# Optimization experiments

Hardware: AMD Instinct MI355X
Metric: run time of the kernel (lower is better)

The kernel has to match this reference:

```python
import jax, jax.numpy as jnp
import numpy as np

N_E = 8192
DIM = 256
BETA = 0.25


def _l2norm(x, eps=1e-12):
    # matches F.normalize(p=2, dim=-1): x / max(||x||, eps)
    n = jnp.sqrt(jnp.sum(x * x, axis=-1, keepdims=True))
    return x / jnp.maximum(n, eps)


def setup_inputs() -> dict:
    key = jax.random.key(0)
    k1, k2 = jax.random.split(key)
    z = jax.random.normal(k1, (8, 1024, DIM), dtype=jnp.float32)
    embedding_weight = jax.random.normal(k2, (N_E, DIM), dtype=jnp.float32)
    return {"z": z, "embedding_weight": embedding_weight}


def reference(z, embedding_weight):
    z = _l2norm(z)                                   # [B,S,D]
    zf = z.reshape(-1, DIM)                          # [N,D]
    embed_norm = _l2norm(embedding_weight)           # [n_e,D]
    # d = ||z||^2 + ||e||^2 - 2 z.e  -> [N, n_e]
    d = (jnp.sum(zf * zf, axis=1, keepdims=True)
         + jnp.sum(embed_norm * embed_norm, axis=1)
         - 2.0 * jnp.einsum('bd,nd->bn', zf, embed_norm))
    encoding_indices = jnp.argmin(d, axis=1).reshape(z.shape[:-1])  # [B,S]
    z_q = embedding_weight[encoding_indices]          # gather raw codes
    z_q = _l2norm(z_q)                                # [B,S,D]
    loss = (BETA * jnp.mean((jax.lax.stop_gradient(z_q) - z) ** 2)
            + jnp.mean((z_q - jax.lax.stop_gradient(z)) ** 2))
    z_q = z + jax.lax.stop_gradient(z_q - z)          # straight-through
    return z_q, loss, encoding_indices
```

## Files before the change

kernel.cpp:

```cpp
#include <hip/hip_runtime.h>
#include <hip/hip_fp16.h>
#include <cfloat>
#include <math.h>

#define DIM    256
#define N_TOK  8192
#define N_E    8192
#define NSEG   1024
#define MARGIN 0.012f

typedef __attribute__((ext_vector_type(8))) short bf16x8;
typedef __attribute__((ext_vector_type(4))) float f32x4;
typedef __attribute__((ext_vector_type(8))) unsigned short ushort8;

__device__ __forceinline__ unsigned short f2bf(float f) {
    unsigned u = __float_as_uint(f);
    unsigned r = u + 0x7fff + ((u >> 16) & 1);
    return (unsigned short)(r >> 16);
}
__device__ __forceinline__ unsigned fkey(float f) {
    unsigned u = __float_as_uint(f);
    return (u & 0x80000000u) ? ~u : (u | 0x80000000u);
}
__device__ __forceinline__ unsigned short f2h(float f) {
    const __half h = __float2half(f);
    return *(const unsigned short*)&h;
}
__device__ __forceinline__ float h2f(unsigned short u) {
    __half_raw r; r.x = u;
    return __half2float((__half)r);
}

__global__ __launch_bounds__(256) void l2norm_all(const float* __restrict__ z,
                                                  const float* __restrict__ emb,
                                                  float* __restrict__ zn,
                                                  unsigned short* __restrict__ zb,
                                                  float* __restrict__ en,
                                                  unsigned short* __restrict__ esw,
                                                  float* __restrict__ e2) {
    const int lane = threadIdx.x & 63;
    const bool isE = blockIdx.x < (N_E / 4);
    const int row = (isE ? blockIdx.x : blockIdx.x - N_E / 4) * 4 + (threadIdx.x >> 6);
    const float* in = isE ? emb : z;
    float* out = isE ? en : zn;
    const float4 v = *(const float4*)(in + row * DIM + lane * 4);
    float s = v.x * v.x + v.y * v.y + v.z * v.z + v.w * v.w;
#pragma unroll
    for (int off = 1; off < 64; off <<= 1) s += __shfl_xor(s, off, 64);
    const float inv = 1.0f / fmaxf(sqrtf(s), 1e-12f);
    const float4 o = make_float4(v.x * inv, v.y * inv, v.z * inv, v.w * inv);
    *(float4*)(out + row * DIM + lane * 4) = o;
    ushort4 ob; ob.x = f2bf(o.x); ob.y = f2bf(o.y); ob.z = f2bf(o.z); ob.w = f2bf(o.w);
    const int k0 = lane * 4;
    if (isE) {
        const size_t sidx = ((size_t)((row >> 4) * 8 + (k0 >> 5)) * 64
                             + ((k0 >> 3) & 3) * 16 + (row & 15)) * 8 + (k0 & 7);
        *(ushort4*)(esw + sidx) = ob;
        float q = o.x * o.x + o.y * o.y + o.z * o.z + o.w * o.w;
#pragma unroll
        for (int off = 1; off < 64; off <<= 1) q += __shfl_xor(q, off, 64);
        if (lane == 0) e2[row] = q;
    } else {
        *(ushort4*)(zb + (size_t)row * DIM + k0) = ob;
    }
}

__global__ __launch_bounds__(256, 2) void mfma_dist(const unsigned short* __restrict__ zb,
                                                    const unsigned short* __restrict__ esw,
                                                    const float* __restrict__ e2,
                                                    unsigned short* __restrict__ segMh) {
    __shared__ __align__(16) unsigned short As[2][128 * 64];
    float* sm = reinterpret_cast<float*>(As);

    const int tid  = threadIdx.x;
    const int lane = tid & 63;
    const int wave = tid >> 6;
    const int wm = wave & 1, wn = wave >> 1;
    const int row0 = (blockIdx.x & 63) * 128;
    const int col0 = (blockIdx.x >> 6) * 128;
    const int fr = lane & 15, q = lane >> 4;

    f32x4 acc[4][4];
#pragma unroll
    for (int ci = 0; ci < 4; ci++)
#pragma unroll
        for (int zi = 0; zi < 4; zi++) acc[ci][zi] = (f32x4){0.f, 0.f, 0.f, 0.f};

    const int aBase = (col0 >> 4) + wn * 4;
    auto la = [&](int i, int kc) {
        return *(const bf16x8*)(esw + (size_t)(aBase + i) * 4096 + kc * 512 + lane * 8);
    };
    const int cxor = (lane & 7) ^ ((lane >> 3) & 7);
    const unsigned short* gZ = zb + (size_t)(row0 + wave * 32 + (lane >> 3)) * DIM + cxor * 8;
    auto stage = [&](int buf, int p) {
#pragma unroll
        for (int j = 0; j < 4; j++) {
            __builtin_amdgcn_global_load_lds(
                (const __attribute__((address_space(1))) unsigned int*)(gZ + (size_t)j * 8 * DIM + p * 64),
                (__attribute__((address_space(3))) unsigned int*)&As[buf][(wave * 32 + j * 8) * 64],
                16, 0, 0);
        }
    };
    auto lz = [&](int buf, int i, int h) {
        const int r = wm * 64 + i * 16 + fr;
        const int slot = (h * 4 + q) ^ (fr & 7);
        return *(const bf16x8*)&As[buf][r * 64 + slot * 8];
    };

    bf16x8 ca[8][4];
#pragma unroll
    for (int i = 0; i < 4; i++) { ca[0][i] = la(i, 0); ca[1][i] = la(i, 1); }
    stage(0, 0);

#pragma unroll
    for (int p = 0; p < 4; p++) {
        __syncthreads();
        if (p < 3) stage((p + 1) & 1, p + 1);
#pragma unroll
        for (int h = 0; h < 2; h++) {
            const int kc = 2 * p + h;
            if (kc + 2 < 8) {
#pragma unroll
                for (int i = 0; i < 4; i++) ca[kc + 2][i] = la(i, kc + 2);
            }
            bf16x8 zfr[4];
#pragma unroll
            for (int i = 0; i < 4; i++) zfr[i] = lz(p & 1, i, h);
#pragma unroll
            for (int ci = 0; ci < 4; ci++)
#pragma unroll
                for (int zi = 0; zi < 4; zi++)
                    acc[ci][zi] = __builtin_amdgcn_mfma_f32_16x16x32_bf16(ca[kc][ci], zfr[zi], acc[ci][zi], 0, 0, 0);
        }
    }

    float4 e2q[4];
#pragma unroll
    for (int ci = 0; ci < 4; ci++)
        e2q[ci] = *(const float4*)&e2[col0 + wn * 64 + ci * 16 + q * 4];
    __syncthreads();
#pragma unroll
    for (int ci = 0; ci < 4; ci++) {
#pragma unroll
        for (int zi = 0; zi < 4; zi++) {
            const float t0 = fmaf(-2.0f, acc[ci][zi][0], e2q[ci].x);
            const float t1 = fmaf(-2.0f, acc[ci][zi][1], e2q[ci].y);
            const float t2 = fmaf(-2.0f, acc[ci][zi][2], e2q[ci].z);
            const float t3 = fmaf(-2.0f, acc[ci][zi][3], e2q[ci].w);
            float mm = fminf(fminf(t0, t1), fminf(t2, t3));
            mm = fminf(mm, __shfl_xor(mm, 16, 64));
            if (q == 0) sm[(wn * 8 + ci * 2 + 0) * 128 + wm * 64 + zi * 16 + fr] = mm;
            if (q == 2) sm[(wn * 8 + ci * 2 + 1) * 128 + wm * 64 + zi * 16 + fr] = mm;
        }
    }
    __syncthreads();
    {
        const int rl = tid & 127, part = tid >> 7;
        ushort8 o8;
#pragma unroll
        for (int j = 0; j < 8; j++) o8[j] = f2h(sm[(part * 8 + j) * 128 + rl]);
        *(ushort8*)&segMh[(size_t)(row0 + rl) * NSEG + (col0 >> 3) + part * 8] = o8;
    }
}

__global__ __launch_bounds__(256) void select_rescore(const unsigned short* __restrict__ segMh,
                                                      const float* __restrict__ en,
                                                      const float* __restrict__ e2,
                                                      float* zq,
                                                      float* out_base,
                                                      float* __restrict__ pl) {
    const int lane = threadIdx.x & 63;
    const int row  = (blockIdx.x << 2) + (threadIdx.x >> 6);
    const unsigned short* ph = segMh + (size_t)row * NSEG + lane * 16;
    const ushort8 u0 = *(const ushort8*)ph;
    const ushort8 u1 = *(const ushort8*)(ph + 8);
    float vv[16];
#pragma unroll
    for (int j = 0; j < 8; j++) { vv[j] = h2f(u0[j]); vv[8 + j] = h2f(u1[j]); }
    float m = vv[0];
#pragma unroll
    for (int j = 1; j < 16; j++) m = fminf(m, vv[j]);
#pragma unroll
    for (int off = 1; off < 64; off <<= 1) m = fminf(m, __shfl_xor(m, off, 64));
    const float thr = m + MARGIN;

    const int q = lane >> 4, f = lane & 15;
    const float4* zp = (const float4*)(zq + (size_t)row * DIM);
    float4 z4[4];
#pragma unroll
    for (int j = 0; j < 4; j++) z4[j] = zp[j * 16 + f];

    unsigned long long pk = ~0ull;
#pragma unroll
    for (int j = 0; j < 16; j++) {
        unsigned long long bal = __ballot(vv[j] <= thr);
        while (bal) {
            const int l = __ffsll(bal) - 1;
            bal &= bal - 1;
            const int seg = l * 16 + j;
#pragma unroll
            for (int g = 0; g < 2; g++) {
                const int col = seg * 8 + g * 4 + q;
                const float4* ep = (const float4*)(en + (size_t)col * DIM);
                float s = 0.f;
#pragma unroll
                for (int jj = 0; jj < 4; jj++) {
                    const float4 ev = ep[jj * 16 + f];
                    s = fmaf(z4[jj].x, ev.x, s); s = fmaf(z4[jj].y, ev.y, s);
                    s = fmaf(z4[jj].z, ev.z, s); s = fmaf(z4[jj].w, ev.w, s);
                }
#pragma unroll
                for (int off = 1; off < 16; off <<= 1) s += __shfl_xor(s, off, 64);
                const float d = fmaf(-2.0f, s, e2[col]);
                const unsigned long long key =
                    ((unsigned long long)fkey(d) << 32) | (unsigned)col;
                if (key < pk) pk = key;
            }
        }
    }
#pragma unroll
    for (int off = 16; off < 64; off <<= 1) {
        const unsigned long long o = __shfl_xor(pk, off, 64);
        if (o < pk) pk = o;
    }
    const int i = (int)(pk & 0xffffffffu);

    const float4 qv = *(const float4*)(en + (size_t)i * DIM + lane * 4);
    const float4 zv = *(const float4*)(zq + (size_t)row * DIM + lane * 4);
    const float dx = qv.x - zv.x, dy = qv.y - zv.y, dz = qv.z - zv.z, dw = qv.w - zv.w;
    float s = dx * dx + dy * dy + dz * dz + dw * dw;
    *(float4*)(zq + (size_t)row * DIM + lane * 4) = qv;
#pragma unroll
    for (int off = 1; off < 64; off <<= 1) s += __shfl_xor(s, off, 64);
    if (lane == 0) {
        pl[row] = s;
        out_base[N_TOK * DIM + 1 + row] = (float)i;
    }
}

__global__ __launch_bounds__(1024) void finalize_loss(const float* __restrict__ pl,
                                                      float* __restrict__ out) {
    __shared__ float sw[16];
    const int t = threadIdx.x;
    float s = 0.f;
#pragma unroll
    for (int j = 0; j < 8; j++) s += pl[t + j * 1024];
#pragma unroll
    for (int off = 1; off < 64; off <<= 1) s += __shfl_xor(s, off, 64);
    if ((t & 63) == 0) sw[t >> 6] = s;
    __syncthreads();
    if (t < 16) {
        float v = sw[t];
#pragma unroll
        for (int off = 1; off < 16; off <<= 1) v += __shfl_xor(v, off, 64);
        if (t == 0) out[N_TOK * DIM] = v * (1.25f / 2097152.0f);
    }
}

extern "C" void kernel_launch(void* const* d_in, const int* in_sizes, int n_in,
                              void* d_out, int out_size, void* d_ws, size_t ws_size,
                              hipStream_t stream) {
    const float* z   = (const float*)d_in[0];
    const float* emb = (const float*)d_in[1];
    float* out = (float*)d_out;
    char* ws = (char*)d_ws;

    float*          en    = (float*)(ws);
    unsigned short* esw   = (unsigned short*)(ws + 8388608);
    unsigned short* zb    = (unsigned short*)(ws + 12582912);
    float*          e2    = (float*)(ws + 16777216);
    unsigned short* segMh = (unsigned short*)(ws + 16809984);
    float*          pl    = (float*)(ws + 33587200);

    l2norm_all<<<(N_E + N_TOK) / 4, 256, 0, stream>>>(z, emb, out, zb, en, esw, e2);
    mfma_dist<<<64 * 64, 256, 0, stream>>>(zb, esw, e2, segMh);
    select_rescore<<<N_TOK / 4, 256, 0, stream>>>(segMh, en, e2, out, out, pl);
    finalize_loss<<<1, 1024, 0, stream>>>(pl, out);
}
```

Baseline: 137.9 us.

## Reuse staged z tile across four codebook column tiles per block

Each block now handles a 128-row z tile against 512 codebook entries, processed as four 128-column sub-tiles, instead of a single 128x128 tile. The z tile's first six K-chunks are loaded into LDS once, and the last two chunks are held in registers. Codebook fragments for the next sub-tile are prefetched while the current one finishes its MFMAs. The grid drops from 4096 to 1024 blocks, which cuts repeated z staging and per-block setup and barriers. The cost is higher register and LDS pressure, which may reduce occupancy, and fewer blocks for latency hiding.

```diff
diff --git a/kernel.cpp b/kernel.cpp
--- a/kernel.cpp
+++ b/kernel.cpp
@@ -69,97 +69,115 @@
                                                     const unsigned short* __restrict__ esw,
                                                     const float* __restrict__ e2,
                                                     unsigned short* __restrict__ segMh) {
-    __shared__ __align__(16) unsigned short As[2][128 * 64];
-    float* sm = reinterpret_cast<float*>(As);
+    __shared__ __align__(16) unsigned short As[6][128][32];
+    __shared__ float smw[4][8][64];
 
     const int tid  = threadIdx.x;
     const int lane = tid & 63;
     const int wave = tid >> 6;
     const int wm = wave & 1, wn = wave >> 1;
-    const int row0 = (blockIdx.x & 63) * 128;
-    const int col0 = (blockIdx.x >> 6) * 128;
+    const int rb = blockIdx.x & 63;
+    const int cb = blockIdx.x >> 6;
+    const int row0 = rb * 128;
     const int fr = lane & 15, q = lane >> 4;
 
-    f32x4 acc[4][4];
-#pragma unroll
-    for (int ci = 0; ci < 4; ci++)
-#pragma unroll
-        for (int zi = 0; zi < 4; zi++) acc[ci][zi] = (f32x4){0.f, 0.f, 0.f, 0.f};
-
-    const int aBase = (col0 >> 4) + wn * 4;
-    auto la = [&](int i, int kc) {
-        return *(const bf16x8*)(esw + (size_t)(aBase + i) * 4096 + kc * 512 + lane * 8);
+    const unsigned short* ebase = esw + (size_t)(cb * 32 + wn * 4) * 4096 + lane * 8;
+    auto la = [&](int ct, int i, int kc) {
+        return *(const bf16x8*)(ebase + (size_t)(ct * 8 + i) * 4096 + kc * 512);
     };
-    const int cxor = (lane & 7) ^ ((lane >> 3) & 7);
-    const unsigned short* gZ = zb + (size_t)(row0 + wave * 32 + (lane >> 3)) * DIM + cxor * 8;
-    auto stage = [&](int buf, int p) {
-#pragma unroll
-        for (int j = 0; j < 4; j++) {
-            __builtin_amdgcn_global_load_lds(
-                (const __attribute__((address_space(1))) unsigned int*)(gZ + (size_t)j * 8 * DIM + p * 64),
-                (__attribute__((address_space(3))) unsigned int*)&As[buf][(wave * 32 + j * 8) * 64],
-                16, 0, 0);
-        }
+    bf16x8 ca[8][4];
+#pragma unroll
+    for (int i = 0; i < 4; i++) ca[0][i] = la(0, i, 0);
+#pragma unroll
+    for (int i = 0; i < 4; i++) ca[1][i] = la(0, i, 1);
+
+    bf16x8 z67[2][4];
+#pragma unroll
+    for (int h = 0; h < 2; h++)
+#pragma unroll
+        for (int i = 0; i < 4; i++)
+            z67[h][i] = *(const bf16x8*)(zb + (size_t)(row0 + wm * 64 + i * 16 + fr) * DIM
+                                         + (6 + h) * 32 + q * 8);
+
+#pragma unroll
+    for (int jj = 0; jj < 12; jj++) {
+        const int idx = wave * 12 + jj;
+        const int kc = idx >> 3, h = idx & 7;
+        __builtin_amdgcn_global_load_lds(
+            (const __attribute__((address_space(1))) unsigned int*)
+                (zb + (size_t)(row0 + h * 16 + (lane >> 2)) * DIM + kc * 32 + (lane & 3) * 8),
+            (__attribute__((address_space(3))) unsigned int*)&As[kc][h * 16][0],
+            16, 0, 0);
+    }
+    __syncthreads();
+
+    const unsigned short* zbase = (const unsigned short*)As + (wm * 64 + fr) * 32 + q * 8;
+    auto lz = [&](int i, int kc) {
+        return *(const bf16x8*)(zbase + kc * 4096 + i * 512);
     };
-    auto lz = [&](int buf, int i, int h) {
-        const int r = wm * 64 + i * 16 + fr;
-        const int slot = (h * 4 + q) ^ (fr & 7);
-        return *(const bf16x8*)&As[buf][r * 64 + slot * 8];
-    };
-
-    bf16x8 ca[8][4];
-#pragma unroll
-    for (int i = 0; i < 4; i++) { ca[0][i] = la(i, 0); ca[1][i] = la(i, 1); }
-    stage(0, 0);
-
-#pragma unroll
-    for (int p = 0; p < 4; p++) {
-        __syncthreads();
-        if (p < 3) stage((p + 1) & 1, p + 1);
-#pragma unroll
-        for (int h = 0; h < 2; h++) {
-            const int kc = 2 * p + h;
-            if (kc + 2 < 8) {
-#pragma unroll
-                for (int i = 0; i < 4; i++) ca[kc + 2][i] = la(i, kc + 2);
-            }
+
+    for (int ct = 0; ct < 4; ++ct) {
+        float4 e2q[4];
+#pragma unroll
+        for (int ci = 0; ci < 4; ci++)
+            e2q[ci] = *(const float4*)&e2[cb * 512 + ct * 128 + wn * 64 + ci * 16 + q * 4];
+
+        f32x4 acc[4][4];
+#pragma unroll
+        for (int ci = 0; ci < 4; ci++)
+#pragma unroll
+            for (int zi = 0; zi < 4; zi++) acc[ci][zi] = (f32x4){0.f, 0.f, 0.f, 0.f};
+
+#pragma unroll
+        for (int kc = 0; kc < 6; kc++) {
+#pragma unroll
+            for (int i = 0; i < 4; i++) ca[kc + 2][i] = la(ct, i, kc + 2);
             bf16x8 zfr[4];
 #pragma unroll
-            for (int i = 0; i < 4; i++) zfr[i] = lz(p & 1, i, h);
+            for (int i = 0; i < 4; i++) zfr[i] = lz(i, kc);
 #pragma unroll
             for (int ci = 0; ci < 4; ci++)
 #pragma unroll
                 for (int zi = 0; zi < 4; zi++)
                     acc[ci][zi] = __builtin_amdgcn_mfma_f32_16x16x32_bf16(ca[kc][ci], zfr[zi], acc[ci][zi], 0, 0, 0);
         }
-    }
-
-    float4 e2q[4];
-#pragma unroll
-    for (int ci = 0; ci < 4; ci++)
-        e2q[ci] = *(const float4*)&e2[col0 + wn * 64 + ci * 16 + q * 4];
-    __syncthreads();
-#pragma unroll
-    for (int ci = 0; ci < 4; ci++) {
-#pragma unroll
-        for (int zi = 0; zi < 4; zi++) {
-            const float t0 = fmaf(-2.0f, acc[ci][zi][0], e2q[ci].x);
-            const float t1 = fmaf(-2.0f, acc[ci][zi][1], e2q[ci].y);
-            const float t2 = fmaf(-2.0f, acc[ci][zi][2], e2q[ci].z);
-            const float t3 = fmaf(-2.0f, acc[ci][zi][3], e2q[ci].w);
-            float mm = fminf(fminf(t0, t1), fminf(t2, t3));
-            mm = fminf(mm, __shfl_xor(mm, 16, 64));
-            if (q == 0) sm[(wn * 8 + ci * 2 + 0) * 128 + wm * 64 + zi * 16 + fr] = mm;
-            if (q == 2) sm[(wn * 8 + ci * 2 + 1) * 128 + wm * 64 + zi * 16 + fr] = mm;
-        }
-    }
-    __syncthreads();
-    {
-        const int rl = tid & 127, part = tid >> 7;
+        if (ct < 3) {
+#pragma unroll
+            for (int i = 0; i < 4; i++) ca[0][i] = la(ct + 1, i, 0);
+        }
+#pragma unroll
+        for (int ci = 0; ci < 4; ci++)
+#pragma unroll
+            for (int zi = 0; zi < 4; zi++)
+                acc[ci][zi] = __builtin_amdgcn_mfma_f32_16x16x32_bf16(ca[6][ci], z67[0][zi], acc[ci][zi], 0, 0, 0);
+        if (ct < 3) {
+#pragma unroll
+            for (int i = 0; i < 4; i++) ca[1][i] = la(ct + 1, i, 1);
+        }
+#pragma unroll
+        for (int ci = 0; ci < 4; ci++)
+#pragma unroll
+            for (int zi = 0; zi < 4; zi++)
+                acc[ci][zi] = __builtin_amdgcn_mfma_f32_16x16x32_bf16(ca[7][ci], z67[1][zi], acc[ci][zi], 0, 0, 0);
+
+#pragma unroll
+        for (int ci = 0; ci < 4; ci++) {
+#pragma unroll
+            for (int zi = 0; zi < 4; zi++) {
+                const float t0 = fmaf(-2.0f, acc[ci][zi][0], e2q[ci].x);
+                const float t1 = fmaf(-2.0f, acc[ci][zi][1], e2q[ci].y);
+                const float t2 = fmaf(-2.0f, acc[ci][zi][2], e2q[ci].z);
+                const float t3 = fmaf(-2.0f, acc[ci][zi][3], e2q[ci].w);
+                float mm = fminf(fminf(t0, t1), fminf(t2, t3));
+                mm = fminf(mm, __shfl_xor(mm, 16, 64));
+                if (q == 0) smw[wave][ci * 2 + 0][zi * 16 + fr] = mm;
+                if (q == 2) smw[wave][ci * 2 + 1][zi * 16 + fr] = mm;
+            }
+        }
         ushort8 o8;
 #pragma unroll
-        for (int j = 0; j < 8; j++) o8[j] = f2h(sm[(part * 8 + j) * 128 + rl]);
-        *(ushort8*)&segMh[(size_t)(row0 + rl) * NSEG + (col0 >> 3) + part * 8] = o8;
+        for (int j = 0; j < 8; j++) o8[j] = f2h(smw[wave][j][lane]);
+        *(ushort8*)&segMh[(size_t)(row0 + wm * 64 + lane) * NSEG + cb * 64 + ct * 16 + wn * 8] = o8;
     }
 }
 
@@ -273,7 +291,7 @@
     float*          pl    = (float*)(ws + 33587200);
 
     l2norm_all<<<(N_E + N_TOK) / 4, 256, 0, stream>>>(z, emb, out, zb, en, esw, e2);
-    mfma_dist<<<64 * 64, 256, 0, stream>>>(zb, esw, e2, segMh);
+    mfma_dist<<<1024, 256, 0, stream>>>(zb, esw, e2, segMh);
     select_rescore<<<N_TOK / 4, 256, 0, stream>>>(segMh, en, e2, out, out, pl);
     finalize_loss<<<1, 1024, 0, stream>>>(pl, out);
 }
```

Result: slower. 214.0 us (+55.2%).

## Drop e2 from MFMA prefilter, relax barriers, pair rescore candidates

Applied to the files above, without the earlier changes.

The MFMA distance kernel now assumes unit code norms, so it no longer loads e2. It replaces __syncthreads with explicit vmcnt waits and raw barriers, and writes segment minima through a per-wave epilogue that needs no block-wide syncs. Its occupancy hint rises to 3 blocks. The rescore loop handles two flagged segments per iteration so more loads are in flight, at the cost of more registers and some redundant work when the count is odd.

```diff
diff --git a/kernel.cpp b/kernel.cpp
--- a/kernel.cpp
+++ b/kernel.cpp
@@ -65,9 +65,8 @@
     }
 }
 
-__global__ __launch_bounds__(256, 2) void mfma_dist(const unsigned short* __restrict__ zb,
+__global__ __launch_bounds__(256, 3) void mfma_dist(const unsigned short* __restrict__ zb,
                                                     const unsigned short* __restrict__ esw,
-                                                    const float* __restrict__ e2,
                                                     unsigned short* __restrict__ segMh) {
     __shared__ __align__(16) unsigned short As[2][128 * 64];
     float* sm = reinterpret_cast<float*>(As);
@@ -108,14 +107,22 @@
     };
 
     bf16x8 ca[8][4];
-#pragma unroll
-    for (int i = 0; i < 4; i++) { ca[0][i] = la(i, 0); ca[1][i] = la(i, 1); }
     stage(0, 0);
+    __builtin_amdgcn_sched_barrier(0);
+#pragma unroll
+    for (int kc = 0; kc < 2; kc++)
+#pragma unroll
+        for (int i = 0; i < 4; i++) ca[kc][i] = la(i, kc);
 
 #pragma unroll
     for (int p = 0; p < 4; p++) {
-        __syncthreads();
-        if (p < 3) stage((p + 1) & 1, p + 1);
+        asm volatile("s_waitcnt vmcnt(8)" ::: "memory");
+        __builtin_amdgcn_s_barrier();
+        __builtin_amdgcn_sched_barrier(0);
+        if (p < 3) {
+            stage((p + 1) & 1, p + 1);
+            __builtin_amdgcn_sched_barrier(0);
+        }
 #pragma unroll
         for (int h = 0; h < 2; h++) {
             const int kc = 2 * p + h;
@@ -134,33 +141,24 @@
         }
     }
 
-    float4 e2q[4];
-#pragma unroll
-    for (int ci = 0; ci < 4; ci++)
-        e2q[ci] = *(const float4*)&e2[col0 + wn * 64 + ci * 16 + q * 4];
-    __syncthreads();
 #pragma unroll
     for (int ci = 0; ci < 4; ci++) {
 #pragma unroll
         for (int zi = 0; zi < 4; zi++) {
-            const float t0 = fmaf(-2.0f, acc[ci][zi][0], e2q[ci].x);
-            const float t1 = fmaf(-2.0f, acc[ci][zi][1], e2q[ci].y);
-            const float t2 = fmaf(-2.0f, acc[ci][zi][2], e2q[ci].z);
-            const float t3 = fmaf(-2.0f, acc[ci][zi][3], e2q[ci].w);
+            const float t0 = fmaf(-2.0f, acc[ci][zi][0], 1.0f);
+            const float t1 = fmaf(-2.0f, acc[ci][zi][1], 1.0f);
+            const float t2 = fmaf(-2.0f, acc[ci][zi][2], 1.0f);
+            const float t3 = fmaf(-2.0f, acc[ci][zi][3], 1.0f);
             float mm = fminf(fminf(t0, t1), fminf(t2, t3));
             mm = fminf(mm, __shfl_xor(mm, 16, 64));
-            if (q == 0) sm[(wn * 8 + ci * 2 + 0) * 128 + wm * 64 + zi * 16 + fr] = mm;
-            if (q == 2) sm[(wn * 8 + ci * 2 + 1) * 128 + wm * 64 + zi * 16 + fr] = mm;
-        }
-    }
-    __syncthreads();
-    {
-        const int rl = tid & 127, part = tid >> 7;
-        ushort8 o8;
-#pragma unroll
-        for (int j = 0; j < 8; j++) o8[j] = f2h(sm[(part * 8 + j) * 128 + rl]);
-        *(ushort8*)&segMh[(size_t)(row0 + rl) * NSEG + (col0 >> 3) + part * 8] = o8;
-    }
+            if (q == 0) sm[wave * 512 + (ci * 2 + 0) * 64 + zi * 16 + fr] = mm;
+            if (q == 2) sm[wave * 512 + (ci * 2 + 1) * 64 + zi * 16 + fr] = mm;
+        }
+    }
+    ushort8 o8;
+#pragma unroll
+    for (int j = 0; j < 8; j++) o8[j] = f2h(sm[wave * 512 + j * 64 + lane]);
+    *(ushort8*)&segMh[(size_t)(row0 + wm * 64 + lane) * NSEG + (col0 >> 3) + wn * 8] = o8;
 }
 
 __global__ __launch_bounds__(256) void select_rescore(const unsigned short* __restrict__ segMh,
@@ -195,27 +193,48 @@
     for (int j = 0; j < 16; j++) {
         unsigned long long bal = __ballot(vv[j] <= thr);
         while (bal) {
-            const int l = __ffsll(bal) - 1;
-            bal &= bal - 1;
-            const int seg = l * 16 + j;
-#pragma unroll
-            for (int g = 0; g < 2; g++) {
-                const int col = seg * 8 + g * 4 + q;
-                const float4* ep = (const float4*)(en + (size_t)col * DIM);
-                float s = 0.f;
-#pragma unroll
-                for (int jj = 0; jj < 4; jj++) {
-                    const float4 ev = ep[jj * 16 + f];
-                    s = fmaf(z4[jj].x, ev.x, s); s = fmaf(z4[jj].y, ev.y, s);
-                    s = fmaf(z4[jj].z, ev.z, s); s = fmaf(z4[jj].w, ev.w, s);
-                }
-#pragma unroll
-                for (int off = 1; off < 16; off <<= 1) s += __shfl_xor(s, off, 64);
-                const float d = fmaf(-2.0f, s, e2[col]);
-                const unsigned long long key =
-                    ((unsigned long long)fkey(d) << 32) | (unsigned)col;
-                if (key < pk) pk = key;
-            }
+            const int l1 = __ffsll(bal) - 1; bal &= bal - 1;
+            int l2 = l1;
+            if (bal) { l2 = __ffsll(bal) - 1; bal &= bal - 1; }
+            const int segA = l1 * 16 + j, segB = l2 * 16 + j;
+            const int cA0 = segA * 8 + q,     cA1 = segA * 8 + 4 + q;
+            const int cB0 = segB * 8 + q,     cB1 = segB * 8 + 4 + q;
+            const float4* pA0 = (const float4*)(en + (size_t)cA0 * DIM);
+            const float4* pA1 = (const float4*)(en + (size_t)cA1 * DIM);
+            const float4* pB0 = (const float4*)(en + (size_t)cB0 * DIM);
+            const float4* pB1 = (const float4*)(en + (size_t)cB1 * DIM);
+            float4 eA0[4], eA1[4], eB0[4], eB1[4];
+#pragma unroll
+            for (int jj = 0; jj < 4; jj++) {
+                eA0[jj] = pA0[jj * 16 + f]; eA1[jj] = pA1[jj * 16 + f];
+                eB0[jj] = pB0[jj * 16 + f]; eB1[jj] = pB1[jj * 16 + f];
+            }
+            float sA0 = 0.f, sA1 = 0.f, sB0 = 0.f, sB1 = 0.f;
+#pragma unroll
+            for (int jj = 0; jj < 4; jj++) {
+                sA0 = fmaf(z4[jj].x, eA0[jj].x, sA0); sA0 = fmaf(z4[jj].y, eA0[jj].y, sA0);
+                sA0 = fmaf(z4[jj].z, eA0[jj].z, sA0); sA0 = fmaf(z4[jj].w, eA0[jj].w, sA0);
+                sA1 = fmaf(z4[jj].x, eA1[jj].x, sA1); sA1 = fmaf(z4[jj].y, eA1[jj].y, sA1);
+                sA1 = fmaf(z4[jj].z, eA1[jj].z, sA1); sA1 = fmaf(z4[jj].w, eA1[jj].w, sA1);
+                sB0 = fmaf(z4[jj].x, eB0[jj].x, sB0); sB0 = fmaf(z4[jj].y, eB0[jj].y, sB0);
+                sB0 = fmaf(z4[jj].z, eB0[jj].z, sB0); sB0 = fmaf(z4[jj].w, eB0[jj].w, sB0);
+                sB1 = fmaf(z4[jj].x, eB1[jj].x, sB1); sB1 = fmaf(z4[jj].y, eB1[jj].y, sB1);
+                sB1 = fmaf(z4[jj].z, eB1[jj].z, sB1); sB1 = fmaf(z4[jj].w, eB1[jj].w, sB1);
+            }
+#pragma unroll
+            for (int off = 1; off < 16; off <<= 1) {
+                sA0 += __shfl_xor(sA0, off, 64); sA1 += __shfl_xor(sA1, off, 64);
+                sB0 += __shfl_xor(sB0, off, 64); sB1 += __shfl_xor(sB1, off, 64);
+            }
+            const float dA0 = fmaf(-2.0f, sA0, e2[cA0]);
+            const float dA1 = fmaf(-2.0f, sA1, e2[cA1]);
+            const float dB0 = fmaf(-2.0f, sB0, e2[cB0]);
+            const float dB1 = fmaf(-2.0f, sB1, e2[cB1]);
+            unsigned long long k;
+            k = ((unsigned long long)fkey(dA0) << 32) | (unsigned)cA0; if (k < pk) pk = k;
+            k = ((unsigned long long)fkey(dA1) << 32) | (unsigned)cA1; if (k < pk) pk = k;
+            k = ((unsigned long long)fkey(dB0) << 32) | (unsigned)cB0; if (k < pk) pk = k;
+            k = ((unsigned long long)fkey(dB1) << 32) | (unsigned)cB1; if (k < pk) pk = k;
         }
     }
 #pragma unroll
@@ -273,7 +292,7 @@
     float*          pl    = (float*)(ws + 33587200);
 
     l2norm_all<<<(N_E + N_TOK) / 4, 256, 0, stream>>>(z, emb, out, zb, en, esw, e2);
-    mfma_dist<<<64 * 64, 256, 0, stream>>>(zb, esw, e2, segMh);
+    mfma_dist<<<64 * 64, 256, 0, stream>>>(zb, esw, segMh);
     select_rescore<<<N_TOK / 4, 256, 0, stream>>>(segMh, en, e2, out, out, pl);
     finalize_loss<<<1, 1024, 0, stream>>>(pl, out);
 }
```

Measured after the change: 137.4 us. No clear change (-0.4%).
